# Performance work log

Measured on AMD Instinct MI355X. Metric: run time of the kernel, lower is better.

The kernel has to match this reference:

```python
import jax, jax.numpy as jnp
import numpy as np

K = 3      # kernel_size
PAD = 1    # (dilation*(K-1)+1)//2 with dilation=1
EPS = 1e-3 # keras BatchNormalization default epsilon


def _unfold(x, k=K, pad=PAD):
    # reflect-pad local-window gather, torch.nn.functional.unfold ordering
    # x: [N,C,H,W] -> [N,C,k*k,H*W]
    N, C, H, W = x.shape
    xp = jnp.pad(x, ((0, 0), (0, 0), (pad, pad), (pad, pad)), mode='reflect')
    pats = jnp.stack([xp[:, :, i:i + H, j:j + W] for i in range(k) for j in range(k)], axis=2)
    return pats.reshape(N, C, k * k, H * W)


def _position(H, W):
    # [1,2,H,W]: channel 0 = x(-1..1 across W), channel 1 = y(-1..1 across H)
    loc_w = jnp.tile(jnp.linspace(-1.0, 1.0, W)[None, :], (H, 1))
    loc_h = jnp.tile(jnp.linspace(-1.0, 1.0, H)[:, None], (1, W))
    return jnp.stack([loc_w, loc_h], axis=0)[None].astype(jnp.float32)


def _bn(x, g, b, m, v):
    # keras BN, default axis=-1 (here the H*W axis), inference mode
    return (x - m) / jnp.sqrt(v + EPS) * g + b


def setup_inputs():
    key = jax.random.key(0)
    ks = jax.random.split(key, 16)
    N, C, H, W = 16, 256, 56, 56
    REL, OUT, SHARE = 16, 64, 8
    HW = H * W
    f = lambda k_, s: jax.random.normal(k_, s, dtype=jnp.float32)
    return {
        'x': f(ks[0], (N, C, H, W)),
        'conv1_w': f(ks[1], (REL, C)) * 0.05,
        'conv2_w': f(ks[2], (REL, C)) * 0.05,
        'conv3_w': f(ks[3], (OUT, C)) * 0.05,
        'convp_w': f(ks[4], (2, 2)),
        'convw1_w': f(ks[5], (REL, REL + 2)) * 0.2,
        'convw2_w': f(ks[6], (OUT // SHARE, REL)) * 0.2,
        'bn1_gamma': 1.0 + 0.1 * f(ks[7], (HW,)),
        'bn1_beta': 0.1 * f(ks[8], (HW,)),
        'bn1_mean': 0.1 * f(ks[9], (HW,)),
        'bn1_var': 1.0 + 0.5 * jax.random.uniform(ks[10], (HW,), dtype=jnp.float32),
        'bn2_gamma': 1.0 + 0.1 * f(ks[11], (HW,)),
        'bn2_beta': 0.1 * f(ks[12], (HW,)),
        'bn2_mean': 0.1 * f(ks[13], (HW,)),
        'bn2_var': 1.0 + 0.5 * jax.random.uniform(ks[14], (HW,), dtype=jnp.float32),
    }


def reference(x, conv1_w, conv2_w, conv3_w, convp_w, convw1_w, convw2_w,
              bn1_gamma, bn1_beta, bn1_mean, bn1_var,
              bn2_gamma, bn2_beta, bn2_mean, bn2_var):
    N, C, H, W = x.shape
    HW = H * W
    # 1x1 convs (channels_first) as channel contractions
    x1 = jnp.einsum('oc,nchw->nohw', conv1_w, x)
    x2 = jnp.einsum('oc,nchw->nohw', conv2_w, x)
    x3 = jnp.einsum('oc,nchw->nohw', conv3_w, x)
    p = jnp.einsum('oc,nchw->nohw', convp_w, _position(H, W))  # [1,2,H,W]
    # subtraction2(x1, x2): center feature minus windowed neighbors -> [N,rel,k^2,HW]
    sub2 = x1.reshape(N, -1, 1, HW) - _unfold(x2)
    # subtraction(p): relative positions -> [1,2,k^2,HW], tiled over batch
    subp = p.reshape(1, 2, 1, HW) - _unfold(p)
    rel = jnp.concatenate([sub2, jnp.tile(subp, (N, 1, 1, 1))], axis=1)  # [N,rel+2,k^2,HW]
    # conv_w: BN -> ReLU -> 1x1 conv -> BN -> ReLU -> 1x1 conv
    h = jax.nn.relu(_bn(rel, bn1_gamma, bn1_beta, bn1_mean, bn1_var))
    h = jnp.einsum('oc,ncjl->nojl', convw1_w, h)
    h = jax.nn.relu(_bn(h, bn2_gamma, bn2_beta, bn2_mean, bn2_var))
    h = jnp.einsum('oc,ncjl->nojl', convw2_w, h)  # [N,out//share,k^2,HW]
    w = jax.nn.softmax(h, axis=-2)                # softmax over the k^2 window axis
    # aggregation: weighted neighbor sum, weight channel shared by share_planes channels
    xu = _unfold(x3)                              # [N,out,k^2,HW]
    c_w = w.shape[1]
    xu = xu.reshape(N, -1, c_w, K * K, HW)        # channel c -> (c//c_w, c%c_w)
    out = jnp.einsum('ncjl,ngcjl->ngcl', w, xu)   # sum over window positions j
    return out.reshape(N, -1, H, W)
```

## Files before the change

### kernel.cpp

```cpp
#include <hip/hip_runtime.h>

typedef short bf16x8 __attribute__((ext_vector_type(8)));
typedef float floatx4 __attribute__((ext_vector_type(4)));
typedef unsigned short ushort4v __attribute__((ext_vector_type(4)));
typedef unsigned int uintx4 __attribute__((ext_vector_type(4)));

#define HW 3136
#define WS 100

#define P_CP   0
#define P_W1   4
#define P_W2   292
#define P_FLAG 420
#define P_BN   424
#define PREP_FLOATS (424 + 4 * HW)

__device__ __forceinline__ unsigned short f2bf(float f) {
    unsigned int u = __float_as_uint(f);
    unsigned int r = (u + 0x7FFFu + ((u >> 16) & 1u)) >> 16;
    return (unsigned short)r;
}
__device__ __forceinline__ float bf2f(unsigned short u) {
    return __uint_as_float(((unsigned int)u) << 16);
}
__device__ __forceinline__ void unp8(uint4 u, float* o) {
    o[0] = bf2f((unsigned short)(u.x & 0xFFFFu)); o[1] = bf2f((unsigned short)(u.x >> 16));
    o[2] = bf2f((unsigned short)(u.y & 0xFFFFu)); o[3] = bf2f((unsigned short)(u.y >> 16));
    o[4] = bf2f((unsigned short)(u.z & 0xFFFFu)); o[5] = bf2f((unsigned short)(u.z >> 16));
    o[6] = bf2f((unsigned short)(u.w & 0xFFFFu)); o[7] = bf2f((unsigned short)(u.w >> 16));
}
__device__ __forceinline__ float ldp(const void* p, int i, int isb) {
    return isb ? bf2f(((const unsigned short*)p)[i]) : ((const float*)p)[i];
}

__device__ __forceinline__ int detect_bf16(const void* varp, int* sflag) {
    if (threadIdx.x == 0) {
        const unsigned short* p = (const unsigned short*)varp;
        int ok = 1;
        for (int i = 0; i < 64; ++i) {
            unsigned short v = p[2 * i];
            if (v < 0x3F80u || v > 0x3FC0u) { ok = 0; break; }
        }
        *sflag = ok;
    }
    __syncthreads();
    return *sflag;
}

struct Stage { unsigned int b[32]; bf16x8 a; };

template <int ISB>
__device__ __forceinline__ void ldstage(const void* x, size_t xb,
                                        const void* wp, int arow, int ch, Stage& s)
{
    if (ISB) {
        const unsigned short* p = (const unsigned short*)x + xb + (size_t)ch * HW;
        #pragma unroll
        for (int j = 0; j < 8; ++j)
            *(uint4*)&s.b[4 * j] = *(const uint4*)(p + (size_t)j * HW);
        s.a = *(const bf16x8*)((const unsigned short*)wp + arow * 256 + ch);
    } else {
        const float* p = (const float*)x + xb + (size_t)ch * HW;
        #pragma unroll
        for (int j = 0; j < 8; ++j) {
            floatx4 f0 = *(const floatx4*)(p + (size_t)j * HW);
            floatx4 f1 = *(const floatx4*)(p + (size_t)j * HW + 4);
            s.b[4 * j + 0] = (unsigned)f2bf(f0[0]) | ((unsigned)f2bf(f0[1]) << 16);
            s.b[4 * j + 1] = (unsigned)f2bf(f0[2]) | ((unsigned)f2bf(f0[3]) << 16);
            s.b[4 * j + 2] = (unsigned)f2bf(f1[0]) | ((unsigned)f2bf(f1[1]) << 16);
            s.b[4 * j + 3] = (unsigned)f2bf(f1[2]) | ((unsigned)f2bf(f1[3]) << 16);
        }
        const float* fp = (const float*)wp + arow * 256 + ch;
        bf16x8 a;
        #pragma unroll
        for (int j = 0; j < 8; ++j) a[j] = (short)f2bf(fp[j]);
        s.a = a;
    }
}

__device__ __forceinline__ void domfma(const Stage& s, floatx4 (&acc)[8])
{
    #pragma unroll
    for (int t = 0; t < 8; ++t) {
        const int wi = t >> 1;
        uintx4 uv;
        #pragma unroll
        for (int d = 0; d < 4; ++d) {
            const unsigned lo = s.b[4 * (2 * d) + wi];
            const unsigned hi = s.b[4 * (2 * d + 1) + wi];
            const unsigned v = (t & 1) ? ((lo >> 16) | (hi & 0xFFFF0000u))
                                       : ((lo & 0xFFFFu) | (hi << 16));
            uv[d] = v;
        }
        bf16x8 B = __builtin_bit_cast(bf16x8, uv);
        acc[t] = __builtin_amdgcn_mfma_f32_16x16x32_bf16(s.a, B, acc[t], 0, 0, 0);
    }
}

template <int ISB>
__device__ void proj_body(const void* x, const void* wp, int arow,
                          size_t xb, int quad, floatx4 (&acc)[8])
{
    Stage s0, s1;
    ldstage<ISB>(x, xb, wp, arow, quad * 8, s0);
    #pragma unroll
    for (int q = 0; q < 8; q += 2) {
        ldstage<ISB>(x, xb, wp, arow, (q + 1) * 32 + quad * 8, s1);
        domfma(s0, acc);
        if (q + 2 < 8)
            ldstage<ISB>(x, xb, wp, arow, (q + 2) * 32 + quad * 8, s0);
        domfma(s1, acc);
    }
}

__global__ __launch_bounds__(192, 2) void proj_kernel(
    const void* __restrict__ x,
    const void* __restrict__ w1, const void* __restrict__ w2,
    const void* __restrict__ w3,
    const void* __restrict__ cpw, const void* __restrict__ cw1,
    const void* __restrict__ cw2,
    const void* __restrict__ b1g, const void* __restrict__ b1b,
    const void* __restrict__ b1m, const void* __restrict__ b1v,
    const void* __restrict__ b2g, const void* __restrict__ b2b,
    const void* __restrict__ b2m, const void* __restrict__ b2v,
    unsigned short* __restrict__ y12,
    unsigned short* __restrict__ y3a,
    float* __restrict__ prep)
{
    __shared__ int sflag;
    const int isb = detect_bf16(b1v, &sflag);
    const int tid = threadIdx.x;

    if (blockIdx.x == 0) {
        for (int i = tid; i < 4;   i += 192) prep[P_CP + i] = ldp(cpw, i, isb);
        for (int i = tid; i < 288; i += 192) prep[P_W1 + i] = ldp(cw1, i, isb);
        for (int i = tid; i < 128; i += 192) prep[P_W2 + i] = ldp(cw2, i, isb);
        if (tid == 0) prep[P_FLAG] = isb ? 1.f : 0.f;
        for (int i = tid; i < HW; i += 192) {
            float a1 = ldp(b1g, i, isb) * rsqrtf(ldp(b1v, i, isb) + 1e-3f);
            float c1 = ldp(b1b, i, isb) - ldp(b1m, i, isb) * a1;
            float a2 = ldp(b2g, i, isb) * rsqrtf(ldp(b2v, i, isb) + 1e-3f);
            float c2 = ldp(b2b, i, isb) - ldp(b2m, i, isb) * a2;
            prep[P_BN + i]          = a1;
            prep[P_BN + HW + i]     = c1;
            prep[P_BN + 2 * HW + i] = a2;
            prep[P_BN + 3 * HW + i] = c2;
        }
    }

    const int b   = blockIdx.x;
    const int n   = b / 50, r = b - n * 50;
    const int rh  = r / 25, pt = r - rh * 25;
    const int px0 = (pt < 24) ? pt * 128 : 3008;
    const int wv  = tid >> 6, lane = tid & 63;
    const int col = lane & 15, quad = lane >> 4;
    const int rt  = rh * 3 + wv;

    const void* wp; int ro;
    if      (rt == 0) { wp = w1; ro = 0;  }
    else if (rt == 1) { wp = w2; ro = 0;  }
    else if (rt == 2) { wp = w3; ro = 0;  }
    else if (rt == 3) { wp = w3; ro = 16; }
    else if (rt == 4) { wp = w3; ro = 32; }
    else              { wp = w3; ro = 48; }

    const size_t xb = (size_t)n * 256 * HW + px0 + 8 * col;

    floatx4 acc[8] = {};
    if (isb) proj_body<1>(x, wp, ro + col, xb, quad, acc);
    else     proj_body<0>(x, wp, ro + col, xb, quad, acc);

    const int chq = quad * 4;
    #pragma unroll
    for (int t = 0; t < 8; ++t) {
        const int px = px0 + 8 * col + t;
        ushort4v pk;
        #pragma unroll
        for (int g = 0; g < 4; ++g) pk[g] = f2bf(acc[t][g]);
        if (rt < 2) {
            *(ushort4v*)(y12 + ((size_t)n * HW + px) * 32 + rt * 16 + chq) = pk;
        } else {
            const int k8 = 2 * (rt - 2) + (quad >> 1);
            *(ushort4v*)(y3a + (((size_t)n * 8 + k8) * HW + px) * 8 + (quad & 1) * 4) = pk;
        }
    }
}

__global__ __launch_bounds__(576) void attn_kernel(
    const unsigned short* __restrict__ y12,
    const unsigned short* __restrict__ y3a,
    const float* __restrict__ prep,
    void* __restrict__ out)
{
    __shared__ float wsm[64 * WS];
    const int tid = threadIdx.x;
    const int blk = blockIdx.x;
    const int n   = blk / 49;
    const int l0  = (blk - n * 49) * 64;
    const int isb = prep[P_FLAG] != 0.f;

    {
        const int j = tid >> 6;
        const int p = tid & 63;
        const int l = l0 + p;
        const int h = l / 56, w = l - h * 56;
        const int dy = j / 3 - 1, dx = j - (j / 3) * 3 - 1;
        int hh = h + dy; hh = (hh < 0) ? -hh : ((hh > 55) ? 110 - hh : hh);
        int ww = w + dx; ww = (ww < 0) ? -ww : ((ww > 55) ? 110 - ww : ww);
        const int nbr = hh * 56 + ww;

        const float a1 = prep[P_BN + l];
        const float c1 = prep[P_BN + HW + l];
        const float a2 = prep[P_BN + 2 * HW + l];
        const float c2 = prep[P_BN + 3 * HW + l];

        const unsigned short* y1p = y12 + ((size_t)n * HW + l) * 32;
        const unsigned short* y2p = y12 + ((size_t)n * HW + nbr) * 32 + 16;
        float y1f[16], y2f[16];
        unp8(*(const uint4*)y1p, y1f);       unp8(*(const uint4*)(y1p + 8), y1f + 8);
        unp8(*(const uint4*)y2p, y2f);       unp8(*(const uint4*)(y2p + 8), y2f + 8);

        float rel[18];
        #pragma unroll
        for (int c = 0; c < 16; ++c)
            rel[c] = fmaxf(fmaf(y1f[c] - y2f[c], a1, c1), 0.f);
        const float dlw = (float)(w - ww) * (2.0f / 55.0f);
        const float dlh = (float)(h - hh) * (2.0f / 55.0f);
        rel[16] = fmaxf(fmaf(prep[P_CP + 0] * dlw + prep[P_CP + 1] * dlh, a1, c1), 0.f);
        rel[17] = fmaxf(fmaf(prep[P_CP + 2] * dlw + prep[P_CP + 3] * dlh, a1, c1), 0.f);

        float h1[16];
        #pragma unroll
        for (int o = 0; o < 16; ++o) {
            float s = 0.f;
            #pragma unroll
            for (int c = 0; c < 18; ++c)
                s = fmaf(prep[P_W1 + o * 18 + c], rel[c], s);
            h1[o] = fmaxf(fmaf(s, a2, c2), 0.f);
        }
        float h2[8];
        #pragma unroll
        for (int o2 = 0; o2 < 8; ++o2) {
            float s = 0.f;
            #pragma unroll
            for (int o = 0; o < 16; ++o)
                s = fmaf(prep[P_W2 + o2 * 16 + o], h1[o], s);
            h2[o2] = s;
        }
        float* wpt = &wsm[p * WS + j * 8];
        *(floatx4*)wpt       = *(floatx4*)&h2[0];
        *(floatx4*)(wpt + 4) = *(floatx4*)&h2[4];
    }
    __syncthreads();

    if (tid < 512) {
        const int c = tid & 7, p = tid >> 3;
        float v[9];
        #pragma unroll
        for (int j = 0; j < 9; ++j) v[j] = wsm[p * WS + j * 8 + c];
        float m = v[0];
        #pragma unroll
        for (int j = 1; j < 9; ++j) m = fmaxf(m, v[j]);
        float s = 0.f;
        #pragma unroll
        for (int j = 0; j < 9; ++j) { v[j] = __expf(v[j] - m); s += v[j]; }
        const float inv = 1.f / s;
        #pragma unroll
        for (int j = 0; j < 9; ++j) wsm[p * WS + j * 8 + c] = v[j] * inv;
    }
    __syncthreads();

    if (tid < 512) {
        const int p  = tid & 63;
        const int k8 = tid >> 6;
        const int l = l0 + p;
        const int h = l / 56, w = l - h * 56;
        int nbr[9];
        #pragma unroll
        for (int dy = 0; dy < 3; ++dy)
            #pragma unroll
            for (int dx = 0; dx < 3; ++dx) {
                int hh = h + dy - 1; hh = (hh < 0) ? -hh : ((hh > 55) ? 110 - hh : hh);
                int ww = w + dx - 1; ww = (ww < 0) ? -ww : ((ww > 55) ? 110 - ww : ww);
                nbr[dy * 3 + dx] = hh * 56 + ww;
            }
        const unsigned short* y3b = y3a + ((size_t)n * 8 + k8) * HW * 8;
        float acc8[8];
        #pragma unroll
        for (int k = 0; k < 8; ++k) acc8[k] = 0.f;
        #pragma unroll
        for (int j = 0; j < 9; ++j) {
            uint4 u = *(const uint4*)(y3b + (size_t)nbr[j] * 8);
            float yv[8];
            unp8(u, yv);
            const float* wpt = &wsm[p * WS + j * 8];
            #pragma unroll
            for (int k = 0; k < 8; ++k)
                acc8[k] = fmaf(wpt[k], yv[k], acc8[k]);
        }
        const size_t obase = ((size_t)n * 64 + k8 * 8) * HW + l;
        #pragma unroll
        for (int k = 0; k < 8; ++k) {
            if (isb) ((unsigned short*)out)[obase + (size_t)k * HW] = f2bf(acc8[k]);
            else     ((float*)out)[obase + (size_t)k * HW]          = acc8[k];
        }
    }
}

extern "C" void kernel_launch(void* const* d_in, const int* in_sizes, int n_in,
                              void* d_out, int out_size, void* d_ws, size_t ws_size,
                              hipStream_t stream)
{
    const size_t y12B = (size_t)16 * HW * 32 * 2;
    const size_t y3aB = (size_t)16 * 8 * HW * 8 * 2;

    unsigned short* y12 = (unsigned short*)d_ws;
    unsigned short* y3a = (unsigned short*)((char*)d_ws + y12B);
    float* prep = (float*)((char*)d_ws + y12B + y3aB);

    proj_kernel<<<dim3(800), dim3(192), 0, stream>>>(
        d_in[0], d_in[1], d_in[2], d_in[3],
        d_in[4], d_in[5], d_in[6],
        d_in[7], d_in[8], d_in[9], d_in[10],
        d_in[11], d_in[12], d_in[13], d_in[14],
        y12, y3a, prep);

    attn_kernel<<<dim3(784), dim3(576), 0, stream>>>(y12, y3a, prep, d_out);
}
```

Before: 156.0 us.

## Halve projection tile width, raise occupancy, and template dtype on host

The projection kernel now gives each block 64 pixels instead of 128, so each lane handles 4 pixels with 4 accumulators. The grid grows to 1568 blocks and the launch bounds allow 4 blocks per CU, which should raise occupancy and latency hiding on the bandwidth-bound 1x1 convolutions. The bf16-versus-fp32 check that read device memory in every block now runs once on the host from the input byte size, and both kernels are templated on the result. In exchange each block does less work per weight load and uses narrower global loads.

```diff
diff --git a/kernel.cpp b/kernel.cpp
--- a/kernel.cpp
+++ b/kernel.cpp
@@ -4,6 +4,7 @@
 typedef float floatx4 __attribute__((ext_vector_type(4)));
 typedef unsigned short ushort4v __attribute__((ext_vector_type(4)));
 typedef unsigned int uintx4 __attribute__((ext_vector_type(4)));
+typedef unsigned int uintx2 __attribute__((ext_vector_type(2)));
 
 #define HW 3136
 #define WS 100
@@ -11,7 +12,6 @@
 #define P_CP   0
 #define P_W1   4
 #define P_W2   292
-#define P_FLAG 420
 #define P_BN   424
 #define PREP_FLOATS (424 + 4 * HW)
 
@@ -33,21 +33,7 @@
     return isb ? bf2f(((const unsigned short*)p)[i]) : ((const float*)p)[i];
 }
 
-__device__ __forceinline__ int detect_bf16(const void* varp, int* sflag) {
-    if (threadIdx.x == 0) {
-        const unsigned short* p = (const unsigned short*)varp;
-        int ok = 1;
-        for (int i = 0; i < 64; ++i) {
-            unsigned short v = p[2 * i];
-            if (v < 0x3F80u || v > 0x3FC0u) { ok = 0; break; }
-        }
-        *sflag = ok;
-    }
-    __syncthreads();
-    return *sflag;
-}
-
-struct Stage { unsigned int b[32]; bf16x8 a; };
+struct __align__(16) Stage { unsigned int b[16]; bf16x8 a; };
 
 template <int ISB>
 __device__ __forceinline__ void ldstage(const void* x, size_t xb,
@@ -57,18 +43,15 @@
         const unsigned short* p = (const unsigned short*)x + xb + (size_t)ch * HW;
         #pragma unroll
         for (int j = 0; j < 8; ++j)
-            *(uint4*)&s.b[4 * j] = *(const uint4*)(p + (size_t)j * HW);
+            *(uintx2*)&s.b[2 * j] = *(const uintx2*)(p + (size_t)j * HW);
         s.a = *(const bf16x8*)((const unsigned short*)wp + arow * 256 + ch);
     } else {
         const float* p = (const float*)x + xb + (size_t)ch * HW;
         #pragma unroll
         for (int j = 0; j < 8; ++j) {
-            floatx4 f0 = *(const floatx4*)(p + (size_t)j * HW);
-            floatx4 f1 = *(const floatx4*)(p + (size_t)j * HW + 4);
-            s.b[4 * j + 0] = (unsigned)f2bf(f0[0]) | ((unsigned)f2bf(f0[1]) << 16);
-            s.b[4 * j + 1] = (unsigned)f2bf(f0[2]) | ((unsigned)f2bf(f0[3]) << 16);
-            s.b[4 * j + 2] = (unsigned)f2bf(f1[0]) | ((unsigned)f2bf(f1[1]) << 16);
-            s.b[4 * j + 3] = (unsigned)f2bf(f1[2]) | ((unsigned)f2bf(f1[3]) << 16);
+            floatx4 f = *(const floatx4*)(p + (size_t)j * HW);
+            s.b[2 * j + 0] = (unsigned)f2bf(f[0]) | ((unsigned)f2bf(f[1]) << 16);
+            s.b[2 * j + 1] = (unsigned)f2bf(f[2]) | ((unsigned)f2bf(f[3]) << 16);
         }
         const float* fp = (const float*)wp + arow * 256 + ch;
         bf16x8 a;
@@ -78,16 +61,16 @@
     }
 }
 
-__device__ __forceinline__ void domfma(const Stage& s, floatx4 (&acc)[8])
+__device__ __forceinline__ void domfma(const Stage& s, floatx4 (&acc)[4])
 {
     #pragma unroll
-    for (int t = 0; t < 8; ++t) {
+    for (int t = 0; t < 4; ++t) {
         const int wi = t >> 1;
         uintx4 uv;
         #pragma unroll
         for (int d = 0; d < 4; ++d) {
-            const unsigned lo = s.b[4 * (2 * d) + wi];
-            const unsigned hi = s.b[4 * (2 * d + 1) + wi];
+            const unsigned lo = s.b[2 * (2 * d) + wi];
+            const unsigned hi = s.b[2 * (2 * d + 1) + wi];
             const unsigned v = (t & 1) ? ((lo >> 16) | (hi & 0xFFFF0000u))
                                        : ((lo & 0xFFFFu) | (hi << 16));
             uv[d] = v;
@@ -99,7 +82,7 @@
 
 template <int ISB>
 __device__ void proj_body(const void* x, const void* wp, int arow,
-                          size_t xb, int quad, floatx4 (&acc)[8])
+                          size_t xb, int quad, floatx4 (&acc)[4])
 {
     Stage s0, s1;
     ldstage<ISB>(x, xb, wp, arow, quad * 8, s0);
@@ -113,7 +96,8 @@
     }
 }
 
-__global__ __launch_bounds__(192, 2) void proj_kernel(
+template <int ISB>
+__global__ __launch_bounds__(192, 4) void proj_kernel(
     const void* __restrict__ x,
     const void* __restrict__ w1, const void* __restrict__ w2,
     const void* __restrict__ w3,
@@ -127,20 +111,17 @@
     unsigned short* __restrict__ y3a,
     float* __restrict__ prep)
 {
-    __shared__ int sflag;
-    const int isb = detect_bf16(b1v, &sflag);
     const int tid = threadIdx.x;
 
     if (blockIdx.x == 0) {
-        for (int i = tid; i < 4;   i += 192) prep[P_CP + i] = ldp(cpw, i, isb);
-        for (int i = tid; i < 288; i += 192) prep[P_W1 + i] = ldp(cw1, i, isb);
-        for (int i = tid; i < 128; i += 192) prep[P_W2 + i] = ldp(cw2, i, isb);
-        if (tid == 0) prep[P_FLAG] = isb ? 1.f : 0.f;
+        for (int i = tid; i < 4;   i += 192) prep[P_CP + i] = ldp(cpw, i, ISB);
+        for (int i = tid; i < 288; i += 192) prep[P_W1 + i] = ldp(cw1, i, ISB);
+        for (int i = tid; i < 128; i += 192) prep[P_W2 + i] = ldp(cw2, i, ISB);
         for (int i = tid; i < HW; i += 192) {
-            float a1 = ldp(b1g, i, isb) * rsqrtf(ldp(b1v, i, isb) + 1e-3f);
-            float c1 = ldp(b1b, i, isb) - ldp(b1m, i, isb) * a1;
-            float a2 = ldp(b2g, i, isb) * rsqrtf(ldp(b2v, i, isb) + 1e-3f);
-            float c2 = ldp(b2b, i, isb) - ldp(b2m, i, isb) * a2;
+            float a1 = ldp(b1g, i, ISB) * rsqrtf(ldp(b1v, i, ISB) + 1e-3f);
+            float c1 = ldp(b1b, i, ISB) - ldp(b1m, i, ISB) * a1;
+            float a2 = ldp(b2g, i, ISB) * rsqrtf(ldp(b2v, i, ISB) + 1e-3f);
+            float c2 = ldp(b2b, i, ISB) - ldp(b2m, i, ISB) * a2;
             prep[P_BN + i]          = a1;
             prep[P_BN + HW + i]     = c1;
             prep[P_BN + 2 * HW + i] = a2;
@@ -149,9 +130,9 @@
     }
 
     const int b   = blockIdx.x;
-    const int n   = b / 50, r = b - n * 50;
-    const int rh  = r / 25, pt = r - rh * 25;
-    const int px0 = (pt < 24) ? pt * 128 : 3008;
+    const int n   = b / 98, r = b - n * 98;
+    const int rh  = r / 49, pt = r - rh * 49;
+    const int px0 = pt * 64;
     const int wv  = tid >> 6, lane = tid & 63;
     const int col = lane & 15, quad = lane >> 4;
     const int rt  = rh * 3 + wv;
@@ -164,16 +145,15 @@
     else if (rt == 4) { wp = w3; ro = 32; }
     else              { wp = w3; ro = 48; }
 
-    const size_t xb = (size_t)n * 256 * HW + px0 + 8 * col;
-
-    floatx4 acc[8] = {};
-    if (isb) proj_body<1>(x, wp, ro + col, xb, quad, acc);
-    else     proj_body<0>(x, wp, ro + col, xb, quad, acc);
+    const size_t xb = (size_t)n * 256 * HW + px0 + 4 * col;
+
+    floatx4 acc[4] = {};
+    proj_body<ISB>(x, wp, ro + col, xb, quad, acc);
 
     const int chq = quad * 4;
     #pragma unroll
-    for (int t = 0; t < 8; ++t) {
-        const int px = px0 + 8 * col + t;
+    for (int t = 0; t < 4; ++t) {
+        const int px = px0 + 4 * col + t;
         ushort4v pk;
         #pragma unroll
         for (int g = 0; g < 4; ++g) pk[g] = f2bf(acc[t][g]);
@@ -186,6 +166,7 @@
     }
 }
 
+template <int ISB>
 __global__ __launch_bounds__(576) void attn_kernel(
     const unsigned short* __restrict__ y12,
     const unsigned short* __restrict__ y3a,
@@ -197,7 +178,6 @@
     const int blk = blockIdx.x;
     const int n   = blk / 49;
     const int l0  = (blk - n * 49) * 64;
-    const int isb = prep[P_FLAG] != 0.f;
 
     {
         const int j = tid >> 6;
@@ -301,7 +281,7 @@
         const size_t obase = ((size_t)n * 64 + k8 * 8) * HW + l;
         #pragma unroll
         for (int k = 0; k < 8; ++k) {
-            if (isb) ((unsigned short*)out)[obase + (size_t)k * HW] = f2bf(acc8[k]);
+            if (ISB) ((unsigned short*)out)[obase + (size_t)k * HW] = f2bf(acc8[k]);
             else     ((float*)out)[obase + (size_t)k * HW]          = acc8[k];
         }
     }
@@ -318,12 +298,23 @@
     unsigned short* y3a = (unsigned short*)((char*)d_ws + y12B);
     float* prep = (float*)((char*)d_ws + y12B + y3aB);
 
-    proj_kernel<<<dim3(800), dim3(192), 0, stream>>>(
-        d_in[0], d_in[1], d_in[2], d_in[3],
-        d_in[4], d_in[5], d_in[6],
-        d_in[7], d_in[8], d_in[9], d_in[10],
-        d_in[11], d_in[12], d_in[13], d_in[14],
-        y12, y3a, prep);
-
-    attn_kernel<<<dim3(784), dim3(576), 0, stream>>>(y12, y3a, prep, d_out);
-}
+    const int isb = (in_sizes[10] == HW * 2);
+
+    if (isb) {
+        proj_kernel<1><<<dim3(1568), dim3(192), 0, stream>>>(
+            d_in[0], d_in[1], d_in[2], d_in[3],
+            d_in[4], d_in[5], d_in[6],
+            d_in[7], d_in[8], d_in[9], d_in[10],
+            d_in[11], d_in[12], d_in[13], d_in[14],
+            y12, y3a, prep);
+        attn_kernel<1><<<dim3(784), dim3(576), 0, stream>>>(y12, y3a, prep, d_out);
+    } else {
+        proj_kernel<0><<<dim3(1568), dim3(192), 0, stream>>>(
+            d_in[0], d_in[1], d_in[2], d_in[3],
+            d_in[4], d_in[5], d_in[6],
+            d_in[7], d_in[8], d_in[9], d_in[10],
+            d_in[11], d_in[12], d_in[13], d_in[14],
+            y12, y3a, prep);
+        attn_kernel<0><<<dim3(784), dim3(576), 0, stream>>>(y12, y3a, prep, d_out);
+    }
+}
```

Result: faster. 150.1 us (-3.8%).
